# Kernel tuning notes

Measured on AMD Instinct MI355X. Metric: run time of the kernel, lower is better.

## Reference

```python
import jax, jax.numpy as jnp
import numpy as np

N_NODES = 8192
N_EDGES = 16384
D = 128          # model_dim
R = 64           # deprel_ext_size
B = 16           # base_size


def setup_inputs() -> dict:
    key = jax.random.key(0)
    k1, k2, k3, k4, k5, k6 = jax.random.split(key, 6)
    inp = jax.random.normal(k1, (N_NODES, D), dtype=jnp.float32)
    deprel_ext_edge = jax.random.randint(k2, (N_EDGES,), 0, R, dtype=jnp.int64)
    edge_index = jax.random.randint(k3, (2, N_EDGES), 0, N_NODES, dtype=jnp.int64)
    # Xavier-uniform-like init scales
    lim_w = float(np.sqrt(6.0 / (D + D)))
    lim_c = float(np.sqrt(6.0 / (R + B)))
    weight = jax.random.uniform(k4, (B, D, D), minval=-lim_w, maxval=lim_w, dtype=jnp.float32)
    w_comp = jax.random.uniform(k5, (R, B), minval=-lim_c, maxval=lim_c, dtype=jnp.float32)
    self_weight = jax.random.uniform(k6, (D, D), minval=-lim_w, maxval=lim_w, dtype=jnp.float32)
    final_bias = jnp.zeros((D,), dtype=jnp.float32)
    return {"inp": inp, "deprel_ext_edge": deprel_ext_edge, "edge_index": edge_index,
            "weight": weight, "w_comp": w_comp, "self_weight": self_weight,
            "final_bias": final_bias}


def reference(inp, deprel_ext_edge, edge_index, weight, w_comp, self_weight, final_bias):
    num_nodes = inp.shape[0]
    # basis decomposition: [R,B] @ [B,D*D] -> [R,D,D]
    full_weight = jnp.einsum('rb,bij->rij', w_comp, weight)
    src = edge_index[0]
    tgt = edge_index[1]
    # per-edge relation weight gather + matvec: [E,D,D], [E,D] -> [E,D]
    filtered_weight = full_weight[deprel_ext_edge]
    filtered_input = inp[src]
    potential_input = jnp.einsum('ei,eij->ej', filtered_input, filtered_weight)
    # neighbor count per (target node, relation) without materializing one-hot:
    # combined index over (node, rel) buckets, segment-sum of ones
    comb = tgt * R + deprel_ext_edge  # [E]
    counts = jax.ops.segment_sum(jnp.ones((comb.shape[0],), dtype=potential_input.dtype),
                                 comb, num_segments=num_nodes * R)
    denumerator = counts[comb][:, None]  # [E,1], always >= 1
    potential_input = potential_input / denumerator
    # scatter-add aggregation into target nodes
    output = jax.ops.segment_sum(potential_input, tgt, num_segments=num_nodes)
    # self-edge projection (nn.Linear: x @ W^T) and final bias
    output = output + inp @ self_weight.T + final_bias
    return output
```

## Files before the change

kernel.cpp:

```cpp
#include <hip/hip_runtime.h>

#define NNODES 8192
#define NEDGES 16384
#define DD 128
#define RR 64
#define BB 16
#define CAP 512
#define ET 11
#define TCAP 20

#define FW_OFF    0
#define CNT_OFF   (RR*DD*DD)
#define RELN_OFF  (CNT_OFF + NNODES*RR)
#define TCNT_OFF  (RELN_OFF + RR)
#define SWT_OFF   (TCNT_OFF + NNODES)
#define SORT_OFF  (SWT_OFF + DD*DD)
#define TLIST_OFF (SORT_OFF + RR*CAP)
#define POT_OFF   (TLIST_OFF + NNODES*TCAP)
#define POTS_OFF  (POT_OFF + NEDGES*DD)

__global__ __launch_bounds__(256) void prep_kernel(
    const float* __restrict__ weight,
    const float* __restrict__ w_comp,
    const float* __restrict__ self_weight,
    const int* __restrict__ deprel,
    const int* __restrict__ edge_index,
    float* __restrict__ ws) {
  const int tid = threadIdx.x, bid = blockIdx.x;
  if (bid < 1024) {
    int r = bid >> 4;
    int ij4 = ((bid & 15) << 8) | tid;
    const float* wc = w_comp + r * BB;
    const float4* w4 = reinterpret_cast<const float4*>(weight);
    float4 acc = {0.f, 0.f, 0.f, 0.f};
#pragma unroll
    for (int b = 0; b < BB; ++b) {
      float c = wc[b];
      float4 v = w4[b * 4096 + ij4];
      acc.x += c * v.x; acc.y += c * v.y; acc.z += c * v.z; acc.w += c * v.w;
    }
    reinterpret_cast<float4*>(ws + FW_OFF)[(r << 12) | ij4] = acc;
  } else if (bid < 1040) {
    int idx = (bid - 1024) * 256 + tid;
    int j = idx >> 5, i0 = (idx & 31) * 4;
    float4 v = *reinterpret_cast<const float4*>(self_weight + j * DD + i0);
    ws[SWT_OFF + (i0 + 0) * DD + j] = v.x;
    ws[SWT_OFF + (i0 + 1) * DD + j] = v.y;
    ws[SWT_OFF + (i0 + 2) * DD + j] = v.z;
    ws[SWT_OFF + (i0 + 3) * DD + j] = v.w;
  } else {
    __shared__ int hist[RR];
    __shared__ int bse[RR];
    int e = (bid - 1040) * 256 + tid;
    int r = deprel[e];
    int t = edge_index[NEDGES + e];
    if (tid < RR) hist[tid] = 0;
    __syncthreads();
    atomicAdd(&hist[r], 1);
    atomicAdd(ws + CNT_OFF + t * RR + r, 1.0f);
    {
      int* tcnt  = reinterpret_cast<int*>(ws + TCNT_OFF);
      int* tlist = reinterpret_cast<int*>(ws + TLIST_OFF);
      int p = atomicAdd(&tcnt[t], 1);
      if (p < TCAP) tlist[t * TCAP + p] = e;
    }
    __syncthreads();
    int* relN = reinterpret_cast<int*>(ws + RELN_OFF);
    if (tid < RR) { bse[tid] = atomicAdd(&relN[tid], hist[tid]); hist[tid] = 0; }
    __syncthreads();
    int p = bse[r] + atomicAdd(&hist[r], 1);
    if (p < CAP) reinterpret_cast<int*>(ws + SORT_OFF)[r * CAP + p] = e;
  }
}

__global__ __launch_bounds__(256, 4) void pot_kernel(
    const float* __restrict__ inp,
    const int* __restrict__ edge_index,
    float* __restrict__ ws) {
  __shared__ __align__(16) float xs[DD * 32];
  __shared__ int eqs[32];
  __shared__ int sqs[32];
  __shared__ float cqs[32];
  const int tid = threadIdx.x;
  const int* relN  = reinterpret_cast<const int*>(ws + RELN_OFF);
  const int* sortE = reinterpret_cast<const int*>(ws + SORT_OFF);
  float* pot  = ws + POT_OFF;
  float* potS = ws + POTS_OFF;

  const int x = blockIdx.x & 7;
  const int k = blockIdx.x >> 3;
  const bool is_edge = k < 8 * ET;
  int r = 0, base = 0, nrem = 32, n0 = 0;
  const float* wsrc;
  if (is_edge) {
    int q = k / ET;
    r = x + 8 * q;
    base = (k - q * ET) * 32;
    int cnt = min(relN[r], ET * 32);
    if (base >= cnt) return;
    nrem = min(32, cnt - base);
    wsrc = ws + FW_OFF + r * DD * DD;
  } else {
    n0 = (x * 32 + (k - 8 * ET)) * 32;
    wsrc = ws + SWT_OFF;
  }

  if (tid < 32) {
    int e = 0, s = 0; float c = 0.f;
    if (is_edge) {
      if (tid < nrem) {
        e = sortE[r * CAP + base + tid];
        s = edge_index[e];
        int t = edge_index[NEDGES + e];
        c = 1.0f / ws[CNT_OFF + t * RR + r];
      }
    } else { s = n0 + tid; c = 1.0f; }
    eqs[tid] = e; sqs[tid] = s; cqs[tid] = c;
  }
  __syncthreads();

  {
    int m = tid & 31, ih = tid >> 5;
    int s = sqs[m]; float c = cqs[m];
    const float4* srcp = reinterpret_cast<const float4*>(inp + s * DD + ih * 16);
#pragma unroll
    for (int kk = 0; kk < 4; ++kk) {
      float4 v = srcp[kk];
      int i = ih * 16 + kk * 4;
      xs[(i + 0) * 32 + m] = v.x * c;
      xs[(i + 1) * 32 + m] = v.y * c;
      xs[(i + 2) * 32 + m] = v.z * c;
      xs[(i + 3) * 32 + m] = v.w * c;
    }
  }
  __syncthreads();

  const int jq = tid & 31, mg = tid >> 5;
  const int j0 = jq * 4, m0 = mg * 4;
  float acc[4][4] = {};
#pragma unroll 8
  for (int i = 0; i < DD; ++i) {
    float4 x4 = *reinterpret_cast<const float4*>(&xs[i * 32 + m0]);
    float4 w4 = *reinterpret_cast<const float4*>(wsrc + i * DD + j0);
    acc[0][0] += x4.x * w4.x; acc[0][1] += x4.x * w4.y; acc[0][2] += x4.x * w4.z; acc[0][3] += x4.x * w4.w;
    acc[1][0] += x4.y * w4.x; acc[1][1] += x4.y * w4.y; acc[1][2] += x4.y * w4.z; acc[1][3] += x4.y * w4.w;
    acc[2][0] += x4.z * w4.x; acc[2][1] += x4.z * w4.y; acc[2][2] += x4.z * w4.z; acc[2][3] += x4.z * w4.w;
    acc[3][0] += x4.w * w4.x; acc[3][1] += x4.w * w4.y; acc[3][2] += x4.w * w4.z; acc[3][3] += x4.w * w4.w;
  }

  if (is_edge) {
#pragma unroll
    for (int mi = 0; mi < 4; ++mi) {
      int mm = m0 + mi;
      if (mm < nrem) {
        float4 o = {acc[mi][0], acc[mi][1], acc[mi][2], acc[mi][3]};
        *reinterpret_cast<float4*>(pot + eqs[mm] * DD + j0) = o;
      }
    }
  } else {
#pragma unroll
    for (int mi = 0; mi < 4; ++mi) {
      float4 o = {acc[mi][0], acc[mi][1], acc[mi][2], acc[mi][3]};
      *reinterpret_cast<float4*>(potS + (n0 + m0 + mi) * DD + j0) = o;
    }
  }
}

__global__ __launch_bounds__(256) void gather_kernel(
    const float* __restrict__ bias,
    const float* __restrict__ ws,
    float* __restrict__ out) {
  const int tid = threadIdx.x;
  const int t = blockIdx.x * 8 + (tid >> 5);
  const int j0 = (tid & 31) * 4;
  const int* tcnt  = reinterpret_cast<const int*>(ws + TCNT_OFF);
  const int* tlist = reinterpret_cast<const int*>(ws + TLIST_OFF) + t * TCAP;
  const float* pot  = ws + POT_OFF;
  const float* potS = ws + POTS_OFF;

  float4 s = *reinterpret_cast<const float4*>(potS + t * DD + j0);
  float4 b4 = *reinterpret_cast<const float4*>(bias + j0);
  s.x += b4.x; s.y += b4.y; s.z += b4.z; s.w += b4.w;
  int deg = tcnt[t];
  deg = min(deg, TCAP);
#pragma unroll 4
  for (int d = 0; d < deg; ++d) {
    int e = tlist[d];
    float4 p = *reinterpret_cast<const float4*>(pot + e * DD + j0);
    s.x += p.x; s.y += p.y; s.z += p.z; s.w += p.w;
  }
  *reinterpret_cast<float4*>(out + t * DD + j0) = s;
}

extern "C" void kernel_launch(void* const* d_in, const int* in_sizes, int n_in,
                              void* d_out, int out_size, void* d_ws, size_t ws_size,
                              hipStream_t stream) {
  const float* inp        = (const float*)d_in[0];
  const int*   deprel     = (const int*)d_in[1];
  const int*   edge_index = (const int*)d_in[2];
  const float* weight     = (const float*)d_in[3];
  const float* w_comp     = (const float*)d_in[4];
  const float* self_w     = (const float*)d_in[5];
  const float* bias       = (const float*)d_in[6];
  float* out = (float*)d_out;
  float* ws  = (float*)d_ws;

  hipMemsetAsync(ws + CNT_OFF, 0,
                 (size_t)(NNODES * RR + RR + NNODES) * sizeof(float), stream);
  prep_kernel<<<1104, 256, 0, stream>>>(weight, w_comp, self_w, deprel, edge_index, ws);
  pot_kernel<<<8 * (8 * ET + 32), 256, 0, stream>>>(inp, edge_index, ws);
  gather_kernel<<<NNODES / 8, 256, 0, stream>>>(bias, ws, out);
}
```

Baseline: 105.1 us.

## Drop count table and fuse self-projection into gather kernel

Removes the NNODES*RR count buffer, including its large memset and per-edge float atomics. Each target's edge list now packs the relation id into high bits, and the gather kernel recomputes each (target, relation) count by scanning that target's short list. The self-weight projection moves out of the pot kernel into the gather kernel as a per-node matvec from shared memory, which removes the potS round trip through global memory. In exchange the gather kernel does more serial work per node: a 128-step FMA loop plus a quadratic scan over the degree.

After: 116.6 us. 10.9% more time.

```diff
diff --git a/kernel.cpp b/kernel.cpp
--- a/kernel.cpp
+++ b/kernel.cpp
@@ -10,14 +10,12 @@
 #define TCAP 20
 
 #define FW_OFF    0
-#define CNT_OFF   (RR*DD*DD)
-#define RELN_OFF  (CNT_OFF + NNODES*RR)
+#define RELN_OFF  (FW_OFF + RR*DD*DD)
 #define TCNT_OFF  (RELN_OFF + RR)
 #define SWT_OFF   (TCNT_OFF + NNODES)
 #define SORT_OFF  (SWT_OFF + DD*DD)
 #define TLIST_OFF (SORT_OFF + RR*CAP)
 #define POT_OFF   (TLIST_OFF + NNODES*TCAP)
-#define POTS_OFF  (POT_OFF + NEDGES*DD)
 
 __global__ __launch_bounds__(256) void prep_kernel(
     const float* __restrict__ weight,
@@ -57,12 +55,11 @@
     if (tid < RR) hist[tid] = 0;
     __syncthreads();
     atomicAdd(&hist[r], 1);
-    atomicAdd(ws + CNT_OFF + t * RR + r, 1.0f);
     {
       int* tcnt  = reinterpret_cast<int*>(ws + TCNT_OFF);
       int* tlist = reinterpret_cast<int*>(ws + TLIST_OFF);
       int p = atomicAdd(&tcnt[t], 1);
-      if (p < TCAP) tlist[t * TCAP + p] = e;
+      if (p < TCAP) tlist[t * TCAP + p] = e | (r << 14);
     }
     __syncthreads();
     int* relN = reinterpret_cast<int*>(ws + RELN_OFF);
@@ -80,57 +77,43 @@
   __shared__ __align__(16) float xs[DD * 32];
   __shared__ int eqs[32];
   __shared__ int sqs[32];
-  __shared__ float cqs[32];
   const int tid = threadIdx.x;
   const int* relN  = reinterpret_cast<const int*>(ws + RELN_OFF);
   const int* sortE = reinterpret_cast<const int*>(ws + SORT_OFF);
-  float* pot  = ws + POT_OFF;
-  float* potS = ws + POTS_OFF;
+  float* pot = ws + POT_OFF;
 
   const int x = blockIdx.x & 7;
   const int k = blockIdx.x >> 3;
-  const bool is_edge = k < 8 * ET;
-  int r = 0, base = 0, nrem = 32, n0 = 0;
-  const float* wsrc;
-  if (is_edge) {
-    int q = k / ET;
-    r = x + 8 * q;
-    base = (k - q * ET) * 32;
-    int cnt = min(relN[r], ET * 32);
-    if (base >= cnt) return;
-    nrem = min(32, cnt - base);
-    wsrc = ws + FW_OFF + r * DD * DD;
-  } else {
-    n0 = (x * 32 + (k - 8 * ET)) * 32;
-    wsrc = ws + SWT_OFF;
-  }
+  const int q = k / ET;
+  const int r = x + 8 * q;
+  const int base = (k - q * ET) * 32;
+  const int cnt = min(relN[r], ET * 32);
+  if (base >= cnt) return;
+  const int nrem = min(32, cnt - base);
+  const float* wsrc = ws + FW_OFF + r * DD * DD;
 
   if (tid < 32) {
-    int e = 0, s = 0; float c = 0.f;
-    if (is_edge) {
-      if (tid < nrem) {
-        e = sortE[r * CAP + base + tid];
-        s = edge_index[e];
-        int t = edge_index[NEDGES + e];
-        c = 1.0f / ws[CNT_OFF + t * RR + r];
-      }
-    } else { s = n0 + tid; c = 1.0f; }
-    eqs[tid] = e; sqs[tid] = s; cqs[tid] = c;
+    int e = 0, s = 0;
+    if (tid < nrem) {
+      e = sortE[r * CAP + base + tid];
+      s = edge_index[e];
+    }
+    eqs[tid] = e; sqs[tid] = s;
   }
   __syncthreads();
 
   {
     int m = tid & 31, ih = tid >> 5;
-    int s = sqs[m]; float c = cqs[m];
+    int s = sqs[m];
     const float4* srcp = reinterpret_cast<const float4*>(inp + s * DD + ih * 16);
 #pragma unroll
     for (int kk = 0; kk < 4; ++kk) {
       float4 v = srcp[kk];
       int i = ih * 16 + kk * 4;
-      xs[(i + 0) * 32 + m] = v.x * c;
-      xs[(i + 1) * 32 + m] = v.y * c;
-      xs[(i + 2) * 32 + m] = v.z * c;
-      xs[(i + 3) * 32 + m] = v.w * c;
+      xs[(i + 0) * 32 + m] = v.x;
+      xs[(i + 1) * 32 + m] = v.y;
+      xs[(i + 2) * 32 + m] = v.z;
+      xs[(i + 3) * 32 + m] = v.w;
     }
   }
   __syncthreads();
@@ -148,46 +131,52 @@
     acc[3][0] += x4.w * w4.x; acc[3][1] += x4.w * w4.y; acc[3][2] += x4.w * w4.z; acc[3][3] += x4.w * w4.w;
   }
 
-  if (is_edge) {
 #pragma unroll
-    for (int mi = 0; mi < 4; ++mi) {
-      int mm = m0 + mi;
-      if (mm < nrem) {
-        float4 o = {acc[mi][0], acc[mi][1], acc[mi][2], acc[mi][3]};
-        *reinterpret_cast<float4*>(pot + eqs[mm] * DD + j0) = o;
-      }
-    }
-  } else {
-#pragma unroll
-    for (int mi = 0; mi < 4; ++mi) {
+  for (int mi = 0; mi < 4; ++mi) {
+    int mm = m0 + mi;
+    if (mm < nrem) {
       float4 o = {acc[mi][0], acc[mi][1], acc[mi][2], acc[mi][3]};
-      *reinterpret_cast<float4*>(potS + (n0 + m0 + mi) * DD + j0) = o;
+      *reinterpret_cast<float4*>(pot + eqs[mm] * DD + j0) = o;
     }
   }
 }
 
 __global__ __launch_bounds__(256) void gather_kernel(
+    const float* __restrict__ inp,
     const float* __restrict__ bias,
     const float* __restrict__ ws,
     float* __restrict__ out) {
+  __shared__ __align__(16) float xrow[8][DD];
   const int tid = threadIdx.x;
-  const int t = blockIdx.x * 8 + (tid >> 5);
-  const int j0 = (tid & 31) * 4;
-  const int* tcnt  = reinterpret_cast<const int*>(ws + TCNT_OFF);
-  const int* tlist = reinterpret_cast<const int*>(ws + TLIST_OFF) + t * TCAP;
-  const float* pot  = ws + POT_OFF;
-  const float* potS = ws + POTS_OFF;
-
-  float4 s = *reinterpret_cast<const float4*>(potS + t * DD + j0);
-  float4 b4 = *reinterpret_cast<const float4*>(bias + j0);
-  s.x += b4.x; s.y += b4.y; s.z += b4.z; s.w += b4.w;
-  int deg = tcnt[t];
-  deg = min(deg, TCAP);
-#pragma unroll 4
+  const int g = tid >> 5, lane = tid & 31;
+  const int t = blockIdx.x * 8 + g;
+  const int j0 = lane * 4;
+
+  *reinterpret_cast<float4*>(&xrow[g][j0]) =
+      *reinterpret_cast<const float4*>(inp + t * DD + j0);
+  __syncthreads();
+
+  const float* swT = ws + SWT_OFF;
+  float4 s = *reinterpret_cast<const float4*>(bias + j0);
+#pragma unroll 8
+  for (int i = 0; i < DD; ++i) {
+    float xv = xrow[g][i];
+    float4 w4 = *reinterpret_cast<const float4*>(swT + i * DD + j0);
+    s.x += xv * w4.x; s.y += xv * w4.y; s.z += xv * w4.z; s.w += xv * w4.w;
+  }
+
+  const int* tcnt = reinterpret_cast<const int*>(ws + TCNT_OFF);
+  const int* tl   = reinterpret_cast<const int*>(ws + TLIST_OFF) + t * TCAP;
+  const float* pot = ws + POT_OFF;
+  int deg = min(tcnt[t], TCAP);
   for (int d = 0; d < deg; ++d) {
-    int e = tlist[d];
+    int pk = tl[d];
+    int e = pk & 16383, rl = pk >> 14;
+    int c = 0;
+    for (int d2 = 0; d2 < deg; ++d2) c += ((tl[d2] >> 14) == rl);
+    float sc = 1.0f / (float)c;
     float4 p = *reinterpret_cast<const float4*>(pot + e * DD + j0);
-    s.x += p.x; s.y += p.y; s.z += p.z; s.w += p.w;
+    s.x += p.x * sc; s.y += p.y * sc; s.z += p.z * sc; s.w += p.w * sc;
   }
   *reinterpret_cast<float4*>(out + t * DD + j0) = s;
 }
@@ -205,9 +194,8 @@
   float* out = (float*)d_out;
   float* ws  = (float*)d_ws;
 
-  hipMemsetAsync(ws + CNT_OFF, 0,
-                 (size_t)(NNODES * RR + RR + NNODES) * sizeof(float), stream);
+  hipMemsetAsync(ws + RELN_OFF, 0, (size_t)(RR + NNODES) * sizeof(float), stream);
   prep_kernel<<<1104, 256, 0, stream>>>(weight, w_comp, self_w, deprel, edge_index, ws);
-  pot_kernel<<<8 * (8 * ET + 32), 256, 0, stream>>>(inp, edge_index, ws);
-  gather_kernel<<<NNODES / 8, 256, 0, stream>>>(bias, ws, out);
-}
+  pot_kernel<<<8 * 8 * ET, 256, 0, stream>>>(inp, edge_index, ws);
+  gather_kernel<<<NNODES / 8, 256, 0, stream>>>(inp, bias, ws, out);
+}
```

## Compute per-relation neighbor counts in gather from packed target lists

Applied to the files above, without the earlier changes.

Removes the dense NNODES*RR count array, its global float atomics and its large memset. Each edge's relation id is packed into the per-target edge list, and the gather kernel counts same-relation neighbors by scanning that short list, then applies the normalization at aggregation time instead of scaling inputs in the matmul kernel. The quadratic scan over at most TCAP entries adds extra list reads per edge. The matmul loop unroll is also raised.

After: 108.8 us. 1.04x slower.

```diff
diff --git a/kernel.cpp b/kernel.cpp
--- a/kernel.cpp
+++ b/kernel.cpp
@@ -10,8 +10,7 @@
 #define TCAP 20
 
 #define FW_OFF    0
-#define CNT_OFF   (RR*DD*DD)
-#define RELN_OFF  (CNT_OFF + NNODES*RR)
+#define RELN_OFF  (FW_OFF + RR*DD*DD)
 #define TCNT_OFF  (RELN_OFF + RR)
 #define SWT_OFF   (TCNT_OFF + NNODES)
 #define SORT_OFF  (SWT_OFF + DD*DD)
@@ -57,12 +56,11 @@
     if (tid < RR) hist[tid] = 0;
     __syncthreads();
     atomicAdd(&hist[r], 1);
-    atomicAdd(ws + CNT_OFF + t * RR + r, 1.0f);
     {
       int* tcnt  = reinterpret_cast<int*>(ws + TCNT_OFF);
       int* tlist = reinterpret_cast<int*>(ws + TLIST_OFF);
       int p = atomicAdd(&tcnt[t], 1);
-      if (p < TCAP) tlist[t * TCAP + p] = e;
+      if (p < TCAP) tlist[t * TCAP + p] = e | (r << 14);
     }
     __syncthreads();
     int* relN = reinterpret_cast<int*>(ws + RELN_OFF);
@@ -80,7 +78,6 @@
   __shared__ __align__(16) float xs[DD * 32];
   __shared__ int eqs[32];
   __shared__ int sqs[32];
-  __shared__ float cqs[32];
   const int tid = threadIdx.x;
   const int* relN  = reinterpret_cast<const int*>(ws + RELN_OFF);
   const int* sortE = reinterpret_cast<const int*>(ws + SORT_OFF);
@@ -106,31 +103,29 @@
   }
 
   if (tid < 32) {
-    int e = 0, s = 0; float c = 0.f;
+    int e = 0, s = 0;
     if (is_edge) {
       if (tid < nrem) {
         e = sortE[r * CAP + base + tid];
         s = edge_index[e];
-        int t = edge_index[NEDGES + e];
-        c = 1.0f / ws[CNT_OFF + t * RR + r];
       }
-    } else { s = n0 + tid; c = 1.0f; }
-    eqs[tid] = e; sqs[tid] = s; cqs[tid] = c;
+    } else { s = n0 + tid; }
+    eqs[tid] = e; sqs[tid] = s;
   }
   __syncthreads();
 
   {
     int m = tid & 31, ih = tid >> 5;
-    int s = sqs[m]; float c = cqs[m];
+    int s = sqs[m];
     const float4* srcp = reinterpret_cast<const float4*>(inp + s * DD + ih * 16);
 #pragma unroll
     for (int kk = 0; kk < 4; ++kk) {
       float4 v = srcp[kk];
       int i = ih * 16 + kk * 4;
-      xs[(i + 0) * 32 + m] = v.x * c;
-      xs[(i + 1) * 32 + m] = v.y * c;
-      xs[(i + 2) * 32 + m] = v.z * c;
-      xs[(i + 3) * 32 + m] = v.w * c;
+      xs[(i + 0) * 32 + m] = v.x;
+      xs[(i + 1) * 32 + m] = v.y;
+      xs[(i + 2) * 32 + m] = v.z;
+      xs[(i + 3) * 32 + m] = v.w;
     }
   }
   __syncthreads();
@@ -138,7 +133,7 @@
   const int jq = tid & 31, mg = tid >> 5;
   const int j0 = jq * 4, m0 = mg * 4;
   float acc[4][4] = {};
-#pragma unroll 8
+#pragma unroll 16
   for (int i = 0; i < DD; ++i) {
     float4 x4 = *reinterpret_cast<const float4*>(&xs[i * 32 + m0]);
     float4 w4 = *reinterpret_cast<const float4*>(wsrc + i * DD + j0);
@@ -173,21 +168,24 @@
   const int tid = threadIdx.x;
   const int t = blockIdx.x * 8 + (tid >> 5);
   const int j0 = (tid & 31) * 4;
-  const int* tcnt  = reinterpret_cast<const int*>(ws + TCNT_OFF);
-  const int* tlist = reinterpret_cast<const int*>(ws + TLIST_OFF) + t * TCAP;
+  const int* tcnt = reinterpret_cast<const int*>(ws + TCNT_OFF);
+  const int* tl   = reinterpret_cast<const int*>(ws + TLIST_OFF) + t * TCAP;
   const float* pot  = ws + POT_OFF;
   const float* potS = ws + POTS_OFF;
 
   float4 s = *reinterpret_cast<const float4*>(potS + t * DD + j0);
   float4 b4 = *reinterpret_cast<const float4*>(bias + j0);
   s.x += b4.x; s.y += b4.y; s.z += b4.z; s.w += b4.w;
-  int deg = tcnt[t];
-  deg = min(deg, TCAP);
-#pragma unroll 4
+
+  int deg = min(tcnt[t], TCAP);
   for (int d = 0; d < deg; ++d) {
-    int e = tlist[d];
+    int pk = tl[d];
+    int e = pk & 16383, rl = pk >> 14;
+    int c = 0;
+    for (int d2 = 0; d2 < deg; ++d2) c += ((tl[d2] >> 14) == rl);
+    float sc = 1.0f / (float)c;
     float4 p = *reinterpret_cast<const float4*>(pot + e * DD + j0);
-    s.x += p.x; s.y += p.y; s.z += p.z; s.w += p.w;
+    s.x += p.x * sc; s.y += p.y * sc; s.z += p.z * sc; s.w += p.w * sc;
   }
   *reinterpret_cast<float4*>(out + t * DD + j0) = s;
 }
@@ -205,8 +203,7 @@
   float* out = (float*)d_out;
   float* ws  = (float*)d_ws;
 
-  hipMemsetAsync(ws + CNT_OFF, 0,
-                 (size_t)(NNODES * RR + RR + NNODES) * sizeof(float), stream);
+  hipMemsetAsync(ws + RELN_OFF, 0, (size_t)(RR + NNODES) * sizeof(float), stream);
   prep_kernel<<<1104, 256, 0, stream>>>(weight, w_comp, self_w, deprel, edge_index, ws);
   pot_kernel<<<8 * (8 * ET + 32), 256, 0, stream>>>(inp, edge_index, ws);
   gather_kernel<<<NNODES / 8, 256, 0, stream>>>(bias, ws, out);
```
